# Kernel tuning notes

Measured on AMD Instinct MI355X. Metric: run time of the kernel, lower is better.

The kernel has to match this reference:

```python
import jax, jax.numpy as jnp
import numpy as np

EPS = 1e-6
SEARCH_RANGE = 4  # K = 2*R+1 = 9


def setup_inputs() -> dict:
    key = jax.random.key(0)
    k1, k2, k3, k4 = jax.random.split(key, 4)
    B, C, H, W = 4, 128, 128, 240
    E = 64
    F_L = jax.random.normal(k1, (B, C, H, W), dtype=jnp.float32)
    F_R = jax.random.normal(k2, (B, C, H, W), dtype=jnp.float32)
    d0 = jax.random.uniform(k3, (B, 1, H, W), dtype=jnp.float32) * 64.0  # pixel disparity
    phi_w = jax.random.normal(k4, (E, C), dtype=jnp.float32) / np.sqrt(C)  # 1x1 conv weight
    return {"F_L": F_L, "F_R": F_R, "d0": d0, "phi_w": phi_w}


def _embed(x, phi_w):
    # 1x1 conv + channel L2 normalize (cosine embedding)
    y = jnp.einsum('ec,bchw->behw', phi_w, x)
    norm = jnp.sqrt(jnp.sum(y * y, axis=1, keepdims=True)) + EPS
    return y / norm


def reference(F_L, F_R, d0, phi_w):
    R = SEARCH_RANGE
    FL = _embed(F_L, phi_w)  # (B,E,H,W)
    FR = _embed(F_R, phi_w)
    B, E, H, W = FL.shape
    deltas = jnp.arange(-R, R + 1, dtype=FL.dtype)  # (K,)
    xx = jnp.arange(W, dtype=FL.dtype)  # base x grid
    # x' = x - (d0 + delta); align_corners=True grid round-trips to pixel coords exactly,
    # y coordinate is identity, so warp is 1D bilinear along W with border clamp.
    xprime = xx[None, None, None, :] - d0[:, None, 0, :, :] - deltas[None, :, None, None]  # (B,K,H,W)
    x0 = jnp.floor(xprime)
    w = xprime - x0  # bilinear weight
    i0 = jnp.clip(x0.astype(jnp.int32), 0, W - 1)
    i1 = jnp.clip(x0.astype(jnp.int32) + 1, 0, W - 1)
    FR_e = FR[:, None]  # (B,1,E,H,W)
    g0 = jnp.take_along_axis(FR_e, i0[:, :, None, :, :], axis=4)  # (B,K,E,H,W)
    g1 = jnp.take_along_axis(FR_e, i1[:, :, None, :, :], axis=4)
    FR_s = g0 * (1.0 - w)[:, :, None] + g1 * w[:, :, None]
    cost_vol = jnp.einsum('behw,bkehw->bkhw', FL, FR_s)  # (B,K,H,W)
    return cost_vol
```

## Files before the change

### kernel.cpp

```cpp
#include <hip/hip_runtime.h>
#include <hip/hip_bf16.h>

#define NB 4
#define NC 128
#define NH 128
#define NW 240
#define NE 64
#define NK 9
#define PLANE (NH*NW)
#define CHW (NC*PLANE)
#define XS 244
#define WS_SIDE ((size_t)NB*NH*NW*64)

typedef __attribute__((ext_vector_type(8))) short short8;
typedef __attribute__((ext_vector_type(4))) float f32x4;
typedef __attribute__((ext_vector_type(2))) __fp16 fp16x2;
typedef __attribute__((ext_vector_type(8))) __fp16 fp16x8;

__device__ __forceinline__ unsigned pk2bf(float x, float y){
  __hip_bfloat162 h = __float22bfloat162_rn(make_float2(x, y));
  return *(unsigned*)&h;
}
__device__ __forceinline__ unsigned short f2bf(float f){
  unsigned u = __float_as_uint(f);
  u += 0x7fffu + ((u>>16)&1u);
  return (unsigned short)(u>>16);
}
__device__ __forceinline__ float bfl(unsigned v){ return __uint_as_float(v<<16); }
__device__ __forceinline__ float bfh(unsigned v){ return __uint_as_float(v & 0xffff0000u); }

__device__ __forceinline__ unsigned pkh(float x, float y){
  fp16x2 h = __builtin_amdgcn_cvt_pkrtz(x, y);
  return __builtin_bit_cast(unsigned, h);
}
__device__ __forceinline__ float fdot2u(unsigned a, unsigned b, float c){
#if __has_builtin(__builtin_amdgcn_fdot2)
  return __builtin_amdgcn_fdot2(__builtin_bit_cast(fp16x2,a),
                                __builtin_bit_cast(fp16x2,b), c, false);
#else
  fp16x2 ha = __builtin_bit_cast(fp16x2,a), hb = __builtin_bit_cast(fp16x2,b);
  return c + (float)ha[0]*(float)hb[0] + (float)ha[1]*(float)hb[1];
#endif
}
__device__ __forceinline__ int swz(int r){ return (r ^ (r>>3)) & 7; }

__global__ __launch_bounds__(512, 4)
void embed_kernel(const float* __restrict__ xL,
                  const float* __restrict__ xR,
                  const float* __restrict__ phig,
                  unsigned short* __restrict__ ws)
{
  __shared__ __attribute__((aligned(16))) unsigned short xs[NC*XS];
  __shared__ __attribute__((aligned(16))) unsigned short phis[NE*136];

  const int tid  = threadIdx.x;
  const int lane = tid & 63;
  const int wv   = tid >> 6;
  const int bid  = blockIdx.x;
  const int side = bid >> 9;
  const int b    = (bid >> 7) & 3;
  const int h    = bid & 127;
  const float* xg = side ? xR : xL;
  unsigned short* outp = ws + (size_t)side * WS_SIDE;
  const size_t base = (size_t)b*CHW + (size_t)h*NW;
  const int pixbase = (b*NH + h)*NW;

  #pragma unroll
  for (int i = 0; i < 4; ++i) {
    int idx = i*512 + tid;
    int e = idx >> 5, q = idx & 31;
    float4 v = *(const float4*)(phig + e*128 + 4*q);
    uint2 pk; pk.x = pkh(v.x, v.y); pk.y = pkh(v.z, v.w);
    *(uint2*)&phis[e*136 + 4*q] = pk;
  }
  #pragma unroll
  for (int i = 0; i < 16; ++i) {
    int tau = i*512 + tid;
    int c = tau >> 6, s = tau & 63;
    if (s < 60) {
      float4 v = *(const float4*)(xg + base + (size_t)c*PLANE + 4*s);
      uint2 pk; pk.x = pkh(v.x, v.y); pk.y = pkh(v.z, v.w);
      *(uint2*)&xs[c*XS + 4*s] = pk;
    }
  }
  __syncthreads();

  const int mrow = lane & 15;
  const int kg   = lane >> 4;

  f32x4 acc[2][4];
  #pragma unroll
  for (int tt = 0; tt < 2; ++tt)
    #pragma unroll
    for (int mt = 0; mt < 4; ++mt) acc[tt][mt] = (f32x4){0.f,0.f,0.f,0.f};
  float inv[2] = {0.f, 0.f};

  #pragma unroll
  for (int tt = 0; tt < 2; ++tt) {
    int nt = wv + 8*tt;
    if (nt < 15) {
      const int col = 16*nt + mrow;
      #pragma unroll
      for (int ks = 0; ks < 4; ++ks) {
        const int r0 = 32*ks + 8*kg;
        fp16x8 bv;
        #pragma unroll
        for (int j = 0; j < 8; ++j)
          bv[j] = *(const __fp16*)&xs[(r0 + j)*XS + col];
        #pragma unroll
        for (int mt = 0; mt < 4; ++mt) {
          short8 raw = *(const short8*)&phis[(16*mt + mrow)*136 + 32*ks + 8*kg];
          fp16x8 af = __builtin_bit_cast(fp16x8, raw);
          acc[tt][mt] = __builtin_amdgcn_mfma_f32_16x16x32_f16(af, bv, acc[tt][mt], 0, 0, 0);
        }
      }
      float ss = 0.f;
      #pragma unroll
      for (int mt = 0; mt < 4; ++mt)
        #pragma unroll
        for (int r = 0; r < 4; ++r)
          ss += acc[tt][mt][r]*acc[tt][mt][r];
      ss += __shfl_xor(ss, 16, 64);
      ss += __shfl_xor(ss, 32, 64);
      inv[tt] = 1.f/(sqrtf(ss) + 1e-6f);
    }
  }
  __syncthreads();

  unsigned short* Ea = &xs[0];
  #pragma unroll
  for (int tt = 0; tt < 2; ++tt) {
    int nt = wv + 8*tt;
    if (nt < 15) {
      int n = 16*nt + mrow;
      #pragma unroll
      for (int mt = 0; mt < 4; ++mt) {
        int e0 = 16*mt + 4*kg;
        uint2 pk;
        pk.x = pkh(acc[tt][mt][0]*inv[tt], acc[tt][mt][1]*inv[tt]);
        pk.y = pkh(acc[tt][mt][2]*inv[tt], acc[tt][mt][3]*inv[tt]);
        int pos = n*64 + ((((e0>>3) ^ (n&7))<<3)) + (e0&7);
        *(uint2*)&Ea[pos] = pk;
      }
    }
  }
  __syncthreads();

  #pragma unroll
  for (int i = 0; i < 4; ++i) {
    int t = i*512 + tid;
    if (t < 1920) {
      int pix = t >> 3, c4 = t & 7;
      uint4 v = *(const uint4*)&Ea[pix*64 + ((c4 ^ (pix&7))<<3)];
      *(uint4*)(outp + (size_t)(pixbase + pix)*64 + c4*8) = v;
    }
  }
}

__global__ __launch_bounds__(512, 4)
void cost_kernel(const unsigned short* __restrict__ ws,
                 const float* __restrict__ d0g,
                 float* __restrict__ outg)
{
  __shared__ __attribute__((aligned(16))) unsigned short FLb[NW*64];
  __shared__ __attribute__((aligned(16))) unsigned short FRb[NW*64];

  const int tid = threadIdx.x;
  const int b   = blockIdx.x >> 7;
  const int h   = blockIdx.x & 127;
  const int pixbase = (b*NH + h)*NW;
  const unsigned short* FLg = ws;
  const unsigned short* FRg = ws + WS_SIDE;

  #pragma unroll
  for (int i = 0; i < 4; ++i) {
    int t = i*512 + tid;
    if (t < 1920) {
      int pix = t >> 3, c4 = t & 7;
      uint4 v = *(const uint4*)(FLg + (size_t)(pixbase + pix)*64 + c4*8);
      *(uint4*)&FLb[pix*64 + ((c4 ^ swz(pix))<<3)] = v;
    }
  }
  #pragma unroll
  for (int i = 0; i < 4; ++i) {
    int t = i*512 + tid;
    if (t < 1920) {
      int pix = t >> 3, c4 = t & 7;
      uint4 v = *(const uint4*)(FRg + (size_t)(pixbase + pix)*64 + c4*8);
      *(uint4*)&FRb[pix*64 + ((c4 ^ swz(pix))<<3)] = v;
    }
  }
  __syncthreads();

  if (tid < 480) {
    const int p  = tid >> 1;
    const int eh = tid & 1;
    float d0v = d0g[pixbase + p];
    float xf  = (float)p - d0v;
    float x0  = floorf(xf);
    float wfr = xf - x0;
    int jb = (int)x0 - 4;

    unsigned fl[16];
    #pragma unroll
    for (int i = 0; i < 4; ++i) {
      int c4 = 4*eh + i;
      uint4 raw = *(const uint4*)&FLb[p*64 + ((c4 ^ swz(p))<<3)];
      fl[4*i+0]=raw.x; fl[4*i+1]=raw.y; fl[4*i+2]=raw.z; fl[4*i+3]=raw.w;
    }

    float D[10];
    #pragma unroll
    for (int t = 0; t < 10; ++t) {
      int j = jb + t;
      j = j < 0 ? 0 : (j > NW-1 ? NW-1 : j);
      float s = 0.f;
      #pragma unroll
      for (int i = 0; i < 4; ++i) {
        int c4 = 4*eh + i;
        uint4 raw = *(const uint4*)&FRb[j*64 + ((c4 ^ swz(j))<<3)];
        s = fdot2u(fl[4*i+0], raw.x, s);
        s = fdot2u(fl[4*i+1], raw.y, s);
        s = fdot2u(fl[4*i+2], raw.z, s);
        s = fdot2u(fl[4*i+3], raw.w, s);
      }
      D[t] = s;
    }
    #pragma unroll
    for (int t = 0; t < 10; ++t) D[t] += __shfl_xor(D[t], 1, 64);

    size_t ob = (size_t)b*NK*PLANE + (size_t)h*NW + p;
    if (eh == 0) {
      #pragma unroll
      for (int k = 0; k < 5; ++k) {
        int t0 = 8 - k;
        outg[ob + (size_t)k*PLANE] = (1.f - wfr)*D[t0] + wfr*D[t0+1];
      }
    } else {
      #pragma unroll
      for (int k = 5; k < 9; ++k) {
        int t0 = 8 - k;
        outg[ob + (size_t)k*PLANE] = (1.f - wfr)*D[t0] + wfr*D[t0+1];
      }
    }
  }
}

__global__ __launch_bounds__(1024, 4)
void corr_kernel(const float* __restrict__ xL,
                 const float* __restrict__ xR,
                 const float* __restrict__ d0g,
                 const float* __restrict__ phig,
                 float* __restrict__ outg)
{
  __shared__ __attribute__((aligned(16))) unsigned short xs[NC*XS];
  __shared__ __attribute__((aligned(16))) unsigned short phis[NE*136];
  __shared__ __attribute__((aligned(16))) unsigned short FLb[NW*64];
  __shared__ __attribute__((aligned(16))) unsigned short FRb[NW*64];

  const int tid  = threadIdx.x;
  const int lane = tid & 63;
  const int wv   = tid >> 6;
  const int b    = blockIdx.x >> 7;
  const int h    = blockIdx.x & 127;
  const size_t base = (size_t)b*CHW + (size_t)h*NW;

  float d0v = 0.f;
  if (tid < NW) d0v = d0g[(b*NH + h)*NW + tid];

  #pragma unroll
  for (int i = 0; i < 2; ++i) {
    int idx = i*1024 + tid;
    int e = idx >> 5, q = idx & 31;
    float4 v = *(const float4*)(phig + e*128 + 4*q);
    uint2 pk; pk.x = pk2bf(v.x, v.y); pk.y = pk2bf(v.z, v.w);
    *(uint2*)&phis[e*136 + 4*q] = pk;
  }

  #pragma unroll
  for (int i = 0; i < 8; ++i) {
    int tau = i*1024 + tid;
    int c = tau >> 6, s = tau & 63;
    if (s < 60) {
      float4 v = *(const float4*)(xL + base + (size_t)c*PLANE + 4*s);
      uint2 pk; pk.x = pk2bf(v.x, v.y); pk.y = pk2bf(v.z, v.w);
      *(uint2*)&xs[c*XS + 4*s] = pk;
    }
  }
  __syncthreads();

  const int mrow = lane & 15;
  const int kg   = lane >> 4;
  const int nt   = wv;

  auto gemm_norm = [&](unsigned short* dst) {
    f32x4 acc[4];
    #pragma unroll
    for (int mt = 0; mt < 4; ++mt) acc[mt] = (f32x4){0.f,0.f,0.f,0.f};

    if (nt < 15) {
      const int col = 16*nt + mrow;
      #pragma unroll
      for (int ks = 0; ks < 4; ++ks) {
        const int r0 = 32*ks + 8*kg;
        short8 bfv;
        #pragma unroll
        for (int j = 0; j < 8; ++j)
          bfv[j] = (short)xs[(r0 + j)*XS + col];
        #pragma unroll
        for (int mt = 0; mt < 4; ++mt) {
          short8 af = *(const short8*)&phis[(16*mt + mrow)*136 + 32*ks + 8*kg];
          acc[mt] = __builtin_amdgcn_mfma_f32_16x16x32_bf16(af, bfv, acc[mt], 0, 0, 0);
        }
      }
      float ss = 0.f;
      #pragma unroll
      for (int mt = 0; mt < 4; ++mt)
        #pragma unroll
        for (int r = 0; r < 4; ++r)
          ss += acc[mt][r]*acc[mt][r];
      ss += __shfl_xor(ss, 16, 64);
      ss += __shfl_xor(ss, 32, 64);
      float inv = 1.f/(sqrtf(ss) + 1e-6f);
      int n = 16*nt + mrow;
      #pragma unroll
      for (int mt = 0; mt < 4; ++mt) {
        int e0 = 16*mt + 4*kg;
        ushort4 pk;
        pk.x = f2bf(acc[mt][0]*inv);
        pk.y = f2bf(acc[mt][1]*inv);
        pk.z = f2bf(acc[mt][2]*inv);
        pk.w = f2bf(acc[mt][3]*inv);
        int pos = n*64 + (((e0>>3) ^ (n&7))<<3) + (e0&7);
        *(ushort4*)&dst[pos] = pk;
      }
    }
  };

  gemm_norm(FLb);
  __syncthreads();

  #pragma unroll
  for (int i = 0; i < 8; ++i) {
    int tau = i*1024 + tid;
    int c = tau >> 6, s = tau & 63;
    if (s < 60) {
      float4 v = *(const float4*)(xR + base + (size_t)c*PLANE + 4*s);
      uint2 pk; pk.x = pk2bf(v.x, v.y); pk.y = pk2bf(v.z, v.w);
      *(uint2*)&xs[c*XS + 4*s] = pk;
    }
  }
  __syncthreads();

  gemm_norm(FRb);
  __syncthreads();

  if (tid < NW) {
    const int p = tid;
    float xf  = (float)p - d0v;
    float x0  = floorf(xf);
    float wfr = xf - x0;
    int jb = (int)x0 - 4;

    float fl[64];
    #pragma unroll
    for (int c = 0; c < 8; ++c) {
      uint4 raw = *(const uint4*)&FLb[p*64 + ((c ^ (p&7))<<3)];
      fl[8*c+0]=bfl(raw.x); fl[8*c+1]=bfh(raw.x);
      fl[8*c+2]=bfl(raw.y); fl[8*c+3]=bfh(raw.y);
      fl[8*c+4]=bfl(raw.z); fl[8*c+5]=bfh(raw.z);
      fl[8*c+6]=bfl(raw.w); fl[8*c+7]=bfh(raw.w);
    }

    float D[10];
    #pragma unroll
    for (int t = 0; t < 10; ++t) {
      int j = jb + t;
      j = j < 0 ? 0 : (j > NW-1 ? NW-1 : j);
      float s = 0.f;
      #pragma unroll
      for (int c = 0; c < 8; ++c) {
        uint4 raw = *(const uint4*)&FRb[j*64 + ((c ^ (j&7))<<3)];
        s += fl[8*c+0]*bfl(raw.x) + fl[8*c+1]*bfh(raw.x)
           + fl[8*c+2]*bfl(raw.y) + fl[8*c+3]*bfh(raw.y)
           + fl[8*c+4]*bfl(raw.z) + fl[8*c+5]*bfh(raw.z)
           + fl[8*c+6]*bfl(raw.w) + fl[8*c+7]*bfh(raw.w);
      }
      D[t] = s;
    }

    size_t ob = (size_t)(b*NK)*PLANE + (size_t)h*NW + p;
    #pragma unroll
    for (int k = 0; k < NK; ++k) {
      int t0 = 8 - k;
      float cv = (1.f - wfr)*D[t0] + wfr*D[t0+1];
      outg[ob + (size_t)k*PLANE] = cv;
    }
  }
}

extern "C" void kernel_launch(void* const* d_in, const int* in_sizes, int n_in,
                              void* d_out, int out_size, void* d_ws, size_t ws_size,
                              hipStream_t stream) {
  const float* xL   = (const float*)d_in[0];
  const float* xR   = (const float*)d_in[1];
  const float* d0g  = (const float*)d_in[2];
  const float* phig = (const float*)d_in[3];
  float* outg = (float*)d_out;

  const size_t need = 2 * WS_SIDE * sizeof(unsigned short);
  if (d_ws != nullptr && ws_size >= need) {
    embed_kernel<<<dim3(2*NB*NH), dim3(512), 0, stream>>>(
        xL, xR, phig, (unsigned short*)d_ws);
    cost_kernel<<<dim3(NB*NH), dim3(512), 0, stream>>>(
        (const unsigned short*)d_ws, d0g, outg);
  } else {
    corr_kernel<<<dim3(NB*NH), dim3(1024), 0, stream>>>(xL, xR, d0g, phig, outg);
  }
}
```

Before: 157.4 us.

## Fuse embedding and cost volume into a single kernel with prefetched right features

Replaces the two-kernel path (embed to a global workspace, then cost) with one fused kernel per image row. The kernel prefetches the right-image features into registers while the left embedding GEMM runs, reuses the xs and phis shared buffers for FR and the output staging, and splits each pixel's dot products across four lanes. Output is staged in shared memory so the global stores are coalesced float4 writes. This removes the bf16 workspace round-trip and the second launch, at the cost of a heavier block (1024 threads, more registers and shared memory) that may limit occupancy.

```diff
diff --git a/kernel.cpp b/kernel.cpp
--- a/kernel.cpp
+++ b/kernel.cpp
@@ -10,24 +10,11 @@
 #define PLANE (NH*NW)
 #define CHW (NC*PLANE)
 #define XS 244
-#define WS_SIDE ((size_t)NB*NH*NW*64)
 
 typedef __attribute__((ext_vector_type(8))) short short8;
 typedef __attribute__((ext_vector_type(4))) float f32x4;
 typedef __attribute__((ext_vector_type(2))) __fp16 fp16x2;
 typedef __attribute__((ext_vector_type(8))) __fp16 fp16x8;
-
-__device__ __forceinline__ unsigned pk2bf(float x, float y){
-  __hip_bfloat162 h = __float22bfloat162_rn(make_float2(x, y));
-  return *(unsigned*)&h;
-}
-__device__ __forceinline__ unsigned short f2bf(float f){
-  unsigned u = __float_as_uint(f);
-  u += 0x7fffu + ((u>>16)&1u);
-  return (unsigned short)(u>>16);
-}
-__device__ __forceinline__ float bfl(unsigned v){ return __uint_as_float(v<<16); }
-__device__ __forceinline__ float bfh(unsigned v){ return __uint_as_float(v & 0xffff0000u); }
 
 __device__ __forceinline__ unsigned pkh(float x, float y){
   fp16x2 h = __builtin_amdgcn_cvt_pkrtz(x, y);
@@ -44,219 +31,16 @@
 }
 __device__ __forceinline__ int swz(int r){ return (r ^ (r>>3)) & 7; }
 
-__global__ __launch_bounds__(512, 4)
-void embed_kernel(const float* __restrict__ xL,
+__global__ __launch_bounds__(1024, 4)
+void fused_kernel(const float* __restrict__ xL,
                   const float* __restrict__ xR,
+                  const float* __restrict__ d0g,
                   const float* __restrict__ phig,
-                  unsigned short* __restrict__ ws)
-{
-  __shared__ __attribute__((aligned(16))) unsigned short xs[NC*XS];
-  __shared__ __attribute__((aligned(16))) unsigned short phis[NE*136];
-
-  const int tid  = threadIdx.x;
-  const int lane = tid & 63;
-  const int wv   = tid >> 6;
-  const int bid  = blockIdx.x;
-  const int side = bid >> 9;
-  const int b    = (bid >> 7) & 3;
-  const int h    = bid & 127;
-  const float* xg = side ? xR : xL;
-  unsigned short* outp = ws + (size_t)side * WS_SIDE;
-  const size_t base = (size_t)b*CHW + (size_t)h*NW;
-  const int pixbase = (b*NH + h)*NW;
-
-  #pragma unroll
-  for (int i = 0; i < 4; ++i) {
-    int idx = i*512 + tid;
-    int e = idx >> 5, q = idx & 31;
-    float4 v = *(const float4*)(phig + e*128 + 4*q);
-    uint2 pk; pk.x = pkh(v.x, v.y); pk.y = pkh(v.z, v.w);
-    *(uint2*)&phis[e*136 + 4*q] = pk;
-  }
-  #pragma unroll
-  for (int i = 0; i < 16; ++i) {
-    int tau = i*512 + tid;
-    int c = tau >> 6, s = tau & 63;
-    if (s < 60) {
-      float4 v = *(const float4*)(xg + base + (size_t)c*PLANE + 4*s);
-      uint2 pk; pk.x = pkh(v.x, v.y); pk.y = pkh(v.z, v.w);
-      *(uint2*)&xs[c*XS + 4*s] = pk;
-    }
-  }
-  __syncthreads();
-
-  const int mrow = lane & 15;
-  const int kg   = lane >> 4;
-
-  f32x4 acc[2][4];
-  #pragma unroll
-  for (int tt = 0; tt < 2; ++tt)
-    #pragma unroll
-    for (int mt = 0; mt < 4; ++mt) acc[tt][mt] = (f32x4){0.f,0.f,0.f,0.f};
-  float inv[2] = {0.f, 0.f};
-
-  #pragma unroll
-  for (int tt = 0; tt < 2; ++tt) {
-    int nt = wv + 8*tt;
-    if (nt < 15) {
-      const int col = 16*nt + mrow;
-      #pragma unroll
-      for (int ks = 0; ks < 4; ++ks) {
-        const int r0 = 32*ks + 8*kg;
-        fp16x8 bv;
-        #pragma unroll
-        for (int j = 0; j < 8; ++j)
-          bv[j] = *(const __fp16*)&xs[(r0 + j)*XS + col];
-        #pragma unroll
-        for (int mt = 0; mt < 4; ++mt) {
-          short8 raw = *(const short8*)&phis[(16*mt + mrow)*136 + 32*ks + 8*kg];
-          fp16x8 af = __builtin_bit_cast(fp16x8, raw);
-          acc[tt][mt] = __builtin_amdgcn_mfma_f32_16x16x32_f16(af, bv, acc[tt][mt], 0, 0, 0);
-        }
-      }
-      float ss = 0.f;
-      #pragma unroll
-      for (int mt = 0; mt < 4; ++mt)
-        #pragma unroll
-        for (int r = 0; r < 4; ++r)
-          ss += acc[tt][mt][r]*acc[tt][mt][r];
-      ss += __shfl_xor(ss, 16, 64);
-      ss += __shfl_xor(ss, 32, 64);
-      inv[tt] = 1.f/(sqrtf(ss) + 1e-6f);
-    }
-  }
-  __syncthreads();
-
-  unsigned short* Ea = &xs[0];
-  #pragma unroll
-  for (int tt = 0; tt < 2; ++tt) {
-    int nt = wv + 8*tt;
-    if (nt < 15) {
-      int n = 16*nt + mrow;
-      #pragma unroll
-      for (int mt = 0; mt < 4; ++mt) {
-        int e0 = 16*mt + 4*kg;
-        uint2 pk;
-        pk.x = pkh(acc[tt][mt][0]*inv[tt], acc[tt][mt][1]*inv[tt]);
-        pk.y = pkh(acc[tt][mt][2]*inv[tt], acc[tt][mt][3]*inv[tt]);
-        int pos = n*64 + ((((e0>>3) ^ (n&7))<<3)) + (e0&7);
-        *(uint2*)&Ea[pos] = pk;
-      }
-    }
-  }
-  __syncthreads();
-
-  #pragma unroll
-  for (int i = 0; i < 4; ++i) {
-    int t = i*512 + tid;
-    if (t < 1920) {
-      int pix = t >> 3, c4 = t & 7;
-      uint4 v = *(const uint4*)&Ea[pix*64 + ((c4 ^ (pix&7))<<3)];
-      *(uint4*)(outp + (size_t)(pixbase + pix)*64 + c4*8) = v;
-    }
-  }
-}
-
-__global__ __launch_bounds__(512, 4)
-void cost_kernel(const unsigned short* __restrict__ ws,
-                 const float* __restrict__ d0g,
-                 float* __restrict__ outg)
-{
-  __shared__ __attribute__((aligned(16))) unsigned short FLb[NW*64];
-  __shared__ __attribute__((aligned(16))) unsigned short FRb[NW*64];
-
-  const int tid = threadIdx.x;
-  const int b   = blockIdx.x >> 7;
-  const int h   = blockIdx.x & 127;
-  const int pixbase = (b*NH + h)*NW;
-  const unsigned short* FLg = ws;
-  const unsigned short* FRg = ws + WS_SIDE;
-
-  #pragma unroll
-  for (int i = 0; i < 4; ++i) {
-    int t = i*512 + tid;
-    if (t < 1920) {
-      int pix = t >> 3, c4 = t & 7;
-      uint4 v = *(const uint4*)(FLg + (size_t)(pixbase + pix)*64 + c4*8);
-      *(uint4*)&FLb[pix*64 + ((c4 ^ swz(pix))<<3)] = v;
-    }
-  }
-  #pragma unroll
-  for (int i = 0; i < 4; ++i) {
-    int t = i*512 + tid;
-    if (t < 1920) {
-      int pix = t >> 3, c4 = t & 7;
-      uint4 v = *(const uint4*)(FRg + (size_t)(pixbase + pix)*64 + c4*8);
-      *(uint4*)&FRb[pix*64 + ((c4 ^ swz(pix))<<3)] = v;
-    }
-  }
-  __syncthreads();
-
-  if (tid < 480) {
-    const int p  = tid >> 1;
-    const int eh = tid & 1;
-    float d0v = d0g[pixbase + p];
-    float xf  = (float)p - d0v;
-    float x0  = floorf(xf);
-    float wfr = xf - x0;
-    int jb = (int)x0 - 4;
-
-    unsigned fl[16];
-    #pragma unroll
-    for (int i = 0; i < 4; ++i) {
-      int c4 = 4*eh + i;
-      uint4 raw = *(const uint4*)&FLb[p*64 + ((c4 ^ swz(p))<<3)];
-      fl[4*i+0]=raw.x; fl[4*i+1]=raw.y; fl[4*i+2]=raw.z; fl[4*i+3]=raw.w;
-    }
-
-    float D[10];
-    #pragma unroll
-    for (int t = 0; t < 10; ++t) {
-      int j = jb + t;
-      j = j < 0 ? 0 : (j > NW-1 ? NW-1 : j);
-      float s = 0.f;
-      #pragma unroll
-      for (int i = 0; i < 4; ++i) {
-        int c4 = 4*eh + i;
-        uint4 raw = *(const uint4*)&FRb[j*64 + ((c4 ^ swz(j))<<3)];
-        s = fdot2u(fl[4*i+0], raw.x, s);
-        s = fdot2u(fl[4*i+1], raw.y, s);
-        s = fdot2u(fl[4*i+2], raw.z, s);
-        s = fdot2u(fl[4*i+3], raw.w, s);
-      }
-      D[t] = s;
-    }
-    #pragma unroll
-    for (int t = 0; t < 10; ++t) D[t] += __shfl_xor(D[t], 1, 64);
-
-    size_t ob = (size_t)b*NK*PLANE + (size_t)h*NW + p;
-    if (eh == 0) {
-      #pragma unroll
-      for (int k = 0; k < 5; ++k) {
-        int t0 = 8 - k;
-        outg[ob + (size_t)k*PLANE] = (1.f - wfr)*D[t0] + wfr*D[t0+1];
-      }
-    } else {
-      #pragma unroll
-      for (int k = 5; k < 9; ++k) {
-        int t0 = 8 - k;
-        outg[ob + (size_t)k*PLANE] = (1.f - wfr)*D[t0] + wfr*D[t0+1];
-      }
-    }
-  }
-}
-
-__global__ __launch_bounds__(1024, 4)
-void corr_kernel(const float* __restrict__ xL,
-                 const float* __restrict__ xR,
-                 const float* __restrict__ d0g,
-                 const float* __restrict__ phig,
-                 float* __restrict__ outg)
+                  float* __restrict__ outg)
 {
   __shared__ __attribute__((aligned(16))) unsigned short xs[NC*XS];
   __shared__ __attribute__((aligned(16))) unsigned short phis[NE*136];
   __shared__ __attribute__((aligned(16))) unsigned short FLb[NW*64];
-  __shared__ __attribute__((aligned(16))) unsigned short FRb[NW*64];
 
   const int tid  = threadIdx.x;
   const int lane = tid & 63;
@@ -264,53 +48,86 @@
   const int b    = blockIdx.x >> 7;
   const int h    = blockIdx.x & 127;
   const size_t base = (size_t)b*CHW + (size_t)h*NW;
-
-  float d0v = 0.f;
-  if (tid < NW) d0v = d0g[(b*NH + h)*NW + tid];
-
+  const int pixbase = (b*NH + h)*NW;
+
+  float d0v = (tid < 960) ? d0g[pixbase + (tid >> 2)] : 0.f;
+
+  float4 xr[8];
+  #pragma unroll
+  for (int i = 0; i < 7; ++i) {
+    unsigned idx = i*1024 + tid;
+    unsigned c = idx / 60u, s = idx - 60u*c;
+    xr[i] = *(const float4*)(xL + base + (size_t)c*PLANE + 4*s);
+  }
+  if (tid < 512) {
+    unsigned idx = 7168 + tid;
+    unsigned c = idx / 60u, s = idx - 60u*c;
+    xr[7] = *(const float4*)(xL + base + (size_t)c*PLANE + 4*s);
+  }
+  float4 pr[2];
   #pragma unroll
   for (int i = 0; i < 2; ++i) {
     int idx = i*1024 + tid;
-    int e = idx >> 5, q = idx & 31;
-    float4 v = *(const float4*)(phig + e*128 + 4*q);
-    uint2 pk; pk.x = pk2bf(v.x, v.y); pk.y = pk2bf(v.z, v.w);
-    *(uint2*)&phis[e*136 + 4*q] = pk;
-  }
-
-  #pragma unroll
-  for (int i = 0; i < 8; ++i) {
-    int tau = i*1024 + tid;
-    int c = tau >> 6, s = tau & 63;
-    if (s < 60) {
-      float4 v = *(const float4*)(xL + base + (size_t)c*PLANE + 4*s);
-      uint2 pk; pk.x = pk2bf(v.x, v.y); pk.y = pk2bf(v.z, v.w);
-      *(uint2*)&xs[c*XS + 4*s] = pk;
-    }
-  }
-  __syncthreads();
+    pr[i] = *(const float4*)(phig + (idx>>5)*128 + 4*(idx&31));
+  }
+  #pragma unroll
+  for (int i = 0; i < 2; ++i) {
+    int idx = i*1024 + tid;
+    uint2 pk; pk.x = pkh(pr[i].x, pr[i].y); pk.y = pkh(pr[i].z, pr[i].w);
+    *(uint2*)&phis[(idx>>5)*136 + 4*(idx&31)] = pk;
+  }
+  #pragma unroll
+  for (int i = 0; i < 7; ++i) {
+    unsigned idx = i*1024 + tid;
+    unsigned c = idx / 60u, s = idx - 60u*c;
+    uint2 pk; pk.x = pkh(xr[i].x, xr[i].y); pk.y = pkh(xr[i].z, xr[i].w);
+    *(uint2*)&xs[c*XS + 4*s] = pk;
+  }
+  if (tid < 512) {
+    unsigned idx = 7168 + tid;
+    unsigned c = idx / 60u, s = idx - 60u*c;
+    uint2 pk; pk.x = pkh(xr[7].x, xr[7].y); pk.y = pkh(xr[7].z, xr[7].w);
+    *(uint2*)&xs[c*XS + 4*s] = pk;
+  }
+  __syncthreads();
+
+  float4 xrR[8];
+  #pragma unroll
+  for (int i = 0; i < 7; ++i) {
+    unsigned idx = i*1024 + tid;
+    unsigned c = idx / 60u, s = idx - 60u*c;
+    xrR[i] = *(const float4*)(xR + base + (size_t)c*PLANE + 4*s);
+  }
+  if (tid < 512) {
+    unsigned idx = 7168 + tid;
+    unsigned c = idx / 60u, s = idx - 60u*c;
+    xrR[7] = *(const float4*)(xR + base + (size_t)c*PLANE + 4*s);
+  }
 
   const int mrow = lane & 15;
   const int kg   = lane >> 4;
   const int nt   = wv;
-
-  auto gemm_norm = [&](unsigned short* dst) {
+  const int n    = 16*nt + mrow;
+
+  uint2 flpk[4];
+  {
     f32x4 acc[4];
     #pragma unroll
     for (int mt = 0; mt < 4; ++mt) acc[mt] = (f32x4){0.f,0.f,0.f,0.f};
-
     if (nt < 15) {
-      const int col = 16*nt + mrow;
+      const int col = n;
       #pragma unroll
       for (int ks = 0; ks < 4; ++ks) {
         const int r0 = 32*ks + 8*kg;
-        short8 bfv;
+        fp16x8 bv;
         #pragma unroll
         for (int j = 0; j < 8; ++j)
-          bfv[j] = (short)xs[(r0 + j)*XS + col];
+          bv[j] = *(const __fp16*)&xs[(r0 + j)*XS + col];
         #pragma unroll
         for (int mt = 0; mt < 4; ++mt) {
-          short8 af = *(const short8*)&phis[(16*mt + mrow)*136 + 32*ks + 8*kg];
-          acc[mt] = __builtin_amdgcn_mfma_f32_16x16x32_bf16(af, bfv, acc[mt], 0, 0, 0);
+          short8 raw = *(const short8*)&phis[(16*mt + mrow)*136 + 32*ks + 8*kg];
+          fp16x8 af = __builtin_bit_cast(fp16x8, raw);
+          acc[mt] = __builtin_amdgcn_mfma_f32_16x16x32_f16(af, bv, acc[mt], 0, 0, 0);
         }
       }
       float ss = 0.f;
@@ -322,54 +139,103 @@
       ss += __shfl_xor(ss, 16, 64);
       ss += __shfl_xor(ss, 32, 64);
       float inv = 1.f/(sqrtf(ss) + 1e-6f);
-      int n = 16*nt + mrow;
       #pragma unroll
       for (int mt = 0; mt < 4; ++mt) {
-        int e0 = 16*mt + 4*kg;
-        ushort4 pk;
-        pk.x = f2bf(acc[mt][0]*inv);
-        pk.y = f2bf(acc[mt][1]*inv);
-        pk.z = f2bf(acc[mt][2]*inv);
-        pk.w = f2bf(acc[mt][3]*inv);
-        int pos = n*64 + (((e0>>3) ^ (n&7))<<3) + (e0&7);
-        *(ushort4*)&dst[pos] = pk;
-      }
-    }
-  };
-
-  gemm_norm(FLb);
-  __syncthreads();
-
-  #pragma unroll
-  for (int i = 0; i < 8; ++i) {
-    int tau = i*1024 + tid;
-    int c = tau >> 6, s = tau & 63;
-    if (s < 60) {
-      float4 v = *(const float4*)(xR + base + (size_t)c*PLANE + 4*s);
-      uint2 pk; pk.x = pk2bf(v.x, v.y); pk.y = pk2bf(v.z, v.w);
-      *(uint2*)&xs[c*XS + 4*s] = pk;
-    }
-  }
-  __syncthreads();
-
-  gemm_norm(FRb);
-  __syncthreads();
-
-  if (tid < NW) {
-    const int p = tid;
+        flpk[mt].x = pkh(acc[mt][0]*inv, acc[mt][1]*inv);
+        flpk[mt].y = pkh(acc[mt][2]*inv, acc[mt][3]*inv);
+      }
+    }
+  }
+  __syncthreads();
+
+  if (nt < 15) {
+    #pragma unroll
+    for (int mt = 0; mt < 4; ++mt) {
+      int e0 = 16*mt + 4*kg;
+      int pos = n*64 + (((e0>>3) ^ swz(n))<<3) + (e0&7);
+      *(uint2*)&FLb[pos] = flpk[mt];
+    }
+  }
+  #pragma unroll
+  for (int i = 0; i < 7; ++i) {
+    unsigned idx = i*1024 + tid;
+    unsigned c = idx / 60u, s = idx - 60u*c;
+    uint2 pk; pk.x = pkh(xrR[i].x, xrR[i].y); pk.y = pkh(xrR[i].z, xrR[i].w);
+    *(uint2*)&xs[c*XS + 4*s] = pk;
+  }
+  if (tid < 512) {
+    unsigned idx = 7168 + tid;
+    unsigned c = idx / 60u, s = idx - 60u*c;
+    uint2 pk; pk.x = pkh(xrR[7].x, xrR[7].y); pk.y = pkh(xrR[7].z, xrR[7].w);
+    *(uint2*)&xs[c*XS + 4*s] = pk;
+  }
+  __syncthreads();
+
+  uint2 frpk[4];
+  {
+    f32x4 acc[4];
+    #pragma unroll
+    for (int mt = 0; mt < 4; ++mt) acc[mt] = (f32x4){0.f,0.f,0.f,0.f};
+    if (nt < 15) {
+      const int col = n;
+      #pragma unroll
+      for (int ks = 0; ks < 4; ++ks) {
+        const int r0 = 32*ks + 8*kg;
+        fp16x8 bv;
+        #pragma unroll
+        for (int j = 0; j < 8; ++j)
+          bv[j] = *(const __fp16*)&xs[(r0 + j)*XS + col];
+        #pragma unroll
+        for (int mt = 0; mt < 4; ++mt) {
+          short8 raw = *(const short8*)&phis[(16*mt + mrow)*136 + 32*ks + 8*kg];
+          fp16x8 af = __builtin_bit_cast(fp16x8, raw);
+          acc[mt] = __builtin_amdgcn_mfma_f32_16x16x32_f16(af, bv, acc[mt], 0, 0, 0);
+        }
+      }
+      float ss = 0.f;
+      #pragma unroll
+      for (int mt = 0; mt < 4; ++mt)
+        #pragma unroll
+        for (int r = 0; r < 4; ++r)
+          ss += acc[mt][r]*acc[mt][r];
+      ss += __shfl_xor(ss, 16, 64);
+      ss += __shfl_xor(ss, 32, 64);
+      float inv = 1.f/(sqrtf(ss) + 1e-6f);
+      #pragma unroll
+      for (int mt = 0; mt < 4; ++mt) {
+        frpk[mt].x = pkh(acc[mt][0]*inv, acc[mt][1]*inv);
+        frpk[mt].y = pkh(acc[mt][2]*inv, acc[mt][3]*inv);
+      }
+    }
+  }
+  __syncthreads();
+
+  unsigned short* FRb = &xs[0];
+  if (nt < 15) {
+    #pragma unroll
+    for (int mt = 0; mt < 4; ++mt) {
+      int e0 = 16*mt + 4*kg;
+      int pos = n*64 + (((e0>>3) ^ swz(n))<<3) + (e0&7);
+      *(uint2*)&FRb[pos] = frpk[mt];
+    }
+  }
+  __syncthreads();
+
+  float* cvb = (float*)phis;
+  if (tid < 960) {
+    const int p  = tid >> 2;
+    const int eh = tid & 3;
     float xf  = (float)p - d0v;
     float x0  = floorf(xf);
     float wfr = xf - x0;
     int jb = (int)x0 - 4;
 
-    float fl[64];
-    #pragma unroll
-    for (int c = 0; c < 8; ++c) {
-      uint4 raw = *(const uint4*)&FLb[p*64 + ((c ^ (p&7))<<3)];
-      fl[8*c+0]=bfl(raw.x); fl[8*c+1]=bfh(raw.x);
-      fl[8*c+2]=bfl(raw.y); fl[8*c+3]=bfh(raw.y);
-      fl[8*c+4]=bfl(raw.z); fl[8*c+5]=bfh(raw.z);
-      fl[8*c+6]=bfl(raw.w); fl[8*c+7]=bfh(raw.w);
+    unsigned fl[8];
+    #pragma unroll
+    for (int i = 0; i < 2; ++i) {
+      int c4 = 2*eh + i;
+      uint4 raw = *(const uint4*)&FLb[p*64 + ((c4 ^ swz(p))<<3)];
+      fl[4*i+0]=raw.x; fl[4*i+1]=raw.y; fl[4*i+2]=raw.z; fl[4*i+3]=raw.w;
     }
 
     float D[10];
@@ -379,23 +245,35 @@
       j = j < 0 ? 0 : (j > NW-1 ? NW-1 : j);
       float s = 0.f;
       #pragma unroll
-      for (int c = 0; c < 8; ++c) {
-        uint4 raw = *(const uint4*)&FRb[j*64 + ((c ^ (j&7))<<3)];
-        s += fl[8*c+0]*bfl(raw.x) + fl[8*c+1]*bfh(raw.x)
-           + fl[8*c+2]*bfl(raw.y) + fl[8*c+3]*bfh(raw.y)
-           + fl[8*c+4]*bfl(raw.z) + fl[8*c+5]*bfh(raw.z)
-           + fl[8*c+6]*bfl(raw.w) + fl[8*c+7]*bfh(raw.w);
+      for (int i = 0; i < 2; ++i) {
+        int c4 = 2*eh + i;
+        uint4 raw = *(const uint4*)&FRb[j*64 + ((c4 ^ swz(j))<<3)];
+        s = fdot2u(fl[4*i+0], raw.x, s);
+        s = fdot2u(fl[4*i+1], raw.y, s);
+        s = fdot2u(fl[4*i+2], raw.z, s);
+        s = fdot2u(fl[4*i+3], raw.w, s);
       }
       D[t] = s;
     }
-
-    size_t ob = (size_t)(b*NK)*PLANE + (size_t)h*NW + p;
-    #pragma unroll
-    for (int k = 0; k < NK; ++k) {
-      int t0 = 8 - k;
-      float cv = (1.f - wfr)*D[t0] + wfr*D[t0+1];
-      outg[ob + (size_t)k*PLANE] = cv;
-    }
+    #pragma unroll
+    for (int t = 0; t < 10; ++t) {
+      D[t] += __shfl_xor(D[t], 1, 64);
+      D[t] += __shfl_xor(D[t], 2, 64);
+    }
+
+    #define WK(k) { const int t0 = 8-(k); cvb[(k)*NW + p] = (1.f - wfr)*D[t0] + wfr*D[t0+1]; }
+    if      (eh == 0) { WK(0) WK(1) WK(2) }
+    else if (eh == 1) { WK(3) WK(4) }
+    else if (eh == 2) { WK(5) WK(6) }
+    else              { WK(7) WK(8) }
+    #undef WK
+  }
+  __syncthreads();
+
+  if (tid < 540) {
+    int k = tid/60, w4 = tid - 60*k;
+    float4 v = *(const float4*)&cvb[k*NW + 4*w4];
+    *(float4*)(outg + (size_t)b*NK*PLANE + (size_t)h*NW + (size_t)k*PLANE + 4*w4) = v;
   }
 }
 
@@ -407,14 +285,5 @@
   const float* d0g  = (const float*)d_in[2];
   const float* phig = (const float*)d_in[3];
   float* outg = (float*)d_out;
-
-  const size_t need = 2 * WS_SIDE * sizeof(unsigned short);
-  if (d_ws != nullptr && ws_size >= need) {
-    embed_kernel<<<dim3(2*NB*NH), dim3(512), 0, stream>>>(
-        xL, xR, phig, (unsigned short*)d_ws);
-    cost_kernel<<<dim3(NB*NH), dim3(512), 0, stream>>>(
-        (const unsigned short*)d_ws, d0g, outg);
-  } else {
-    corr_kernel<<<dim3(NB*NH), dim3(1024), 0, stream>>>(xL, xR, d0g, phig, outg);
-  }
-}
+  fused_kernel<<<dim3(NB*NH), dim3(1024), 0, stream>>>(xL, xR, d0g, phig, outg);
+}
```

Result: faster. 153.6 us (-2.4%).
